# Kernel optimization log

Measured on AMD Instinct MI355X. Metric: run time of the kernel, lower is better.

The kernel has to match this reference:

```python
import jax, jax.numpy as jnp
import numpy as np

MAX_GRAD = 200.0
N_BLOCKS = 8

@jax.custom_jvp
def sqrt_bound(x):
    return jnp.sqrt(x)

@sqrt_bound.defjvp
def _sqrt_bound_jvp(primals, tangents):
    (x,), (xd,) = primals, tangents
    clipped = jnp.maximum(x, 1.0 / (4.0 * MAX_GRAD * MAX_GRAD))
    return jnp.sqrt(x), xd / (2.0 * jnp.sqrt(clipped))

def block_diag_linear(x, W, b):
    # x: [B,S,Din], W: [n_blocks, Din/n, Dout/n], b: [Dout]
    B, S, Din = x.shape
    n, blk_in, blk_out = W.shape
    xb = x.reshape(B, S, n, blk_in)
    y = jnp.einsum('bsnh,nhd->bsnd', xb, W).reshape(B, S, n * blk_out)
    return y + b

def _scan_combine(c1, c2):
    a1r, a1i, x1r, x1i = c1
    a2r, a2i, x2r, x2i = c2
    ar = a2r * a1r - a2i * a1i
    ai = a2r * a1i + a2i * a1r
    xr = a2r * x1r - a2i * x1i + x2r
    xi = a2r * x1i + a2i * x1r + x2i
    return (ar, ai, xr, xi)

def rglru_forward(x, a_real_param, a_imag_param, W_in, b_in, Wg_x, bg_x, Wg_a, bg_a, W_out, b_out):
    # x: [B, S, d_in]
    x_h = jnp.einsum('bsd,dh->bsh', x, W_in) + b_in          # [B,S,d_hidden]
    gate_x = jax.nn.sigmoid(block_diag_linear(x_h, Wg_x, bg_x))  # [B,S,Dh]
    gate_a = jax.nn.sigmoid(block_diag_linear(x_h, Wg_a, bg_a))  # [B,S,Dh]
    log_a = -8.0 * gate_a * jax.nn.softplus(a_real_param)        # Re(log a)
    log_a_imag = a_imag_param * gate_a                           # Im(log a)
    mag = jnp.exp(log_a)
    a_re = mag * jnp.cos(log_a_imag)
    a_im = mag * jnp.sin(log_a_imag)
    a_sq = jnp.exp(2.0 * log_a)                                  # |a|^2
    Dh = log_a.shape[-1]
    # merged_to_complex: first half -> real part, second half -> imag part
    xr = x_h[..., :Dh]
    xi = x_h[..., Dh:]
    xr = gate_x * xr
    xi = gate_x * xi
    norm = sqrt_bound(1.0 - a_sq)                                # input normalization
    xr = norm * xr
    xi = norm * xi
    # linear recurrence h_t = a_t * h_{t-1} + x_t  (h0 = 0), parallel scan over seq axis
    _, _, hr, hi = jax.lax.associative_scan(_scan_combine, (a_re, a_im, xr, xi), axis=1)
    h = jnp.concatenate([hr, hi], axis=-1)                       # complex_to_merged
    h_last = jnp.concatenate([hr[:, -1], hi[:, -1]], axis=-1)    # [B, d_hidden]
    y = jnp.einsum('bsh,hd->bsd', h, W_out) + b_out              # Dense(d_in)
    return y, h_last

def setup_inputs() -> dict:
    key = jax.random.key(0)
    ks = jax.random.split(key, 10)
    B, S, d_in, d_hidden = 4, 4096, 2048, 2048
    Dh = d_hidden // 2
    blk_in, blk_out = d_hidden // N_BLOCKS, Dh // N_BLOCKS
    r_min, r_max, max_imag, eps = 0.9, 0.999, 0.1, 1e-8
    u1 = jax.random.uniform(ks[0], (Dh,))
    a_real = 0.5 * jnp.log(u1 * (r_max**2 - r_min**2) + r_min**2 + eps)
    a_real_param = jnp.log(jnp.exp(-a_real) - 1.0)
    a_imag_param = jnp.pi * max_imag * jax.random.uniform(ks[1], (Dh,))
    x = jax.random.normal(ks[2], (B, S, d_in), dtype=jnp.float32)
    W_in = jax.random.normal(ks[3], (d_in, d_hidden)) / np.sqrt(d_in)
    Wg_x = jax.random.normal(ks[4], (N_BLOCKS, blk_in, blk_out)) / np.sqrt(blk_in)
    Wg_a = jax.random.normal(ks[5], (N_BLOCKS, blk_in, blk_out)) / np.sqrt(blk_in)
    W_out = jax.random.normal(ks[6], (d_hidden, d_in)) / np.sqrt(d_hidden)
    return {
        'x': x,
        'a_real_param': a_real_param.astype(jnp.float32),
        'a_imag_param': a_imag_param.astype(jnp.float32),
        'W_in': W_in.astype(jnp.float32), 'b_in': jnp.zeros((d_hidden,), jnp.float32),
        'Wg_x': Wg_x.astype(jnp.float32), 'bg_x': jnp.zeros((Dh,), jnp.float32),
        'Wg_a': Wg_a.astype(jnp.float32), 'bg_a': jnp.zeros((Dh,), jnp.float32),
        'W_out': W_out.astype(jnp.float32), 'b_out': jnp.zeros((d_in,), jnp.float32),
    }

def reference(x, a_real_param, a_imag_param, W_in, b_in, Wg_x, bg_x, Wg_a, bg_a, W_out, b_out):
    return rglru_forward(x, a_real_param, a_imag_param, W_in, b_in, Wg_x, bg_x, Wg_a, bg_a, W_out, b_out)
```

## Files before the change

kernel.cpp:

```cpp
#include <hip/hip_runtime.h>
#include <hip/hip_bf16.h>


typedef unsigned short u16;
typedef unsigned int u32;
typedef __attribute__((ext_vector_type(8))) short short8;
typedef __attribute__((ext_vector_type(4))) float floatx4;

#define DEV __device__ __forceinline__

DEV float bf2f(u16 u) { union { u32 i; float f; } v; v.i = ((u32)u) << 16; return v.f; }
DEV u16 f2bf(float f) {
  union { float f; u32 i; } v; v.f = f;
  u32 r = v.i + 0x7fffu + ((v.i >> 16) & 1u);
  return (u16)(r >> 16);
}
DEV float sigmoidf_(float x) { return 1.f / (1.f + __expf(-x)); }

template <typename T> DEV T toOut(float v);
template <> DEV u16 toOut<u16>(float v) { return f2bf(v); }
template <> DEV float toOut<float>(float v) { return v; }

#if __has_builtin(__builtin_amdgcn_global_load_lds)
#define USE_ASYNC_LDS 1
#endif

DEV void cp16(const void* g, void* l) {
#if defined(USE_ASYNC_LDS) && defined(__HIP_DEVICE_COMPILE__)
  __builtin_amdgcn_global_load_lds((const __attribute__((address_space(1))) u32*)g,
                                   (__attribute__((address_space(3))) u32*)l, 16, 0, 0);
#else
  *(short8*)l = *(const short8*)g;
#endif
}
#define WAIT_VM() asm volatile("s_waitcnt vmcnt(0)" ::: "memory")

__global__ __launch_bounds__(256) void convert_f32_bf16(
    const float* __restrict__ src, u16* __restrict__ dst, long n) {
  long i = ((long)blockIdx.x * 256 + threadIdx.x) * 8;
  if (i >= n) return;
  float4 a = *(const float4*)(src + i);
  float4 b = *(const float4*)(src + i + 4);
  union { u16 u[8]; short8 v; } o;
  o.u[0] = f2bf(a.x); o.u[1] = f2bf(a.y); o.u[2] = f2bf(a.z); o.u[3] = f2bf(a.w);
  o.u[4] = f2bf(b.x); o.u[5] = f2bf(b.y); o.u[6] = f2bf(b.z); o.u[7] = f2bf(b.w);
  *(short8*)(dst + i) = o.v;
}

__global__ __launch_bounds__(256) void transpose_f32_bf16(
    const float* __restrict__ src, u16* __restrict__ dst, int R, int C,
    long sBatch, long dBatch) {
  __shared__ u16 tile[32][33];
  const int n = blockIdx.z;
  src += (long)n * sBatch;
  dst += (long)n * dBatch;
  const int c0 = blockIdx.x * 32, r0 = blockIdx.y * 32;
  const int tx = threadIdx.x, ty = threadIdx.y;
#pragma unroll
  for (int i = 0; i < 32; i += 8)
    tile[ty + i][tx] = f2bf(src[(long)(r0 + ty + i) * C + c0 + tx]);
  __syncthreads();
#pragma unroll
  for (int i = 0; i < 32; i += 8) dst[(long)(c0 + ty + i) * R + r0 + tx] = tile[tx][ty + i];
}

template <typename OutT>
__global__ __launch_bounds__(256) void gemm_bt_bias(
    const u16* __restrict__ A, const u16* __restrict__ BT,
    const float* __restrict__ bias, OutT* __restrict__ C, int M, int N, int K) {
  __shared__ __align__(16) u16 As[128 * 64];
  __shared__ __align__(16) u16 Bs[128 * 64];
  const int mt = M >> 7;
  const int bm = blockIdx.x % mt, bn = blockIdx.x / mt;
  const int m0 = bm << 7, n0 = bn << 7;
  const int tid = threadIdx.x;
  const int lane = tid & 63, wid = tid >> 6;
  const int wm = (wid & 1) << 6, wn = (wid >> 1) << 6;
  const int lq = lane >> 4, lm = lane & 15;

  floatx4 acc[4][4];
#pragma unroll
  for (int i = 0; i < 4; ++i)
#pragma unroll
    for (int j = 0; j < 4; ++j) { acc[i][j].x = 0.f; acc[i][j].y = 0.f; acc[i][j].z = 0.f; acc[i][j].w = 0.f; }

  for (int kt = 0; kt < K; kt += 64) {
#pragma unroll
    for (int j = 0; j < 4; ++j) {
      int slot = (j << 8) + tid;
      int row = slot >> 3, ch = slot & 7;
      int gch = ch ^ (row & 7);
      cp16(A + (size_t)(m0 + row) * K + kt + (gch << 3), (char*)As + slot * 16);
    }
#pragma unroll
    for (int j = 0; j < 4; ++j) {
      int slot = (j << 8) + tid;
      int row = slot >> 3, ch = slot & 7;
      int gch = ch ^ (row & 7);
      cp16(BT + (size_t)(n0 + row) * K + kt + (gch << 3), (char*)Bs + slot * 16);
    }
    WAIT_VM();
    __syncthreads();
#pragma unroll
    for (int kk = 0; kk < 64; kk += 32) {
      const int lc = (kk >> 3) + lq;
      short8 af[4], bfr[4];
#pragma unroll
      for (int mi = 0; mi < 4; ++mi) {
        int r = wm + mi * 16 + lm;
        af[mi] = *(const short8*)&As[r * 64 + ((lc ^ (r & 7)) << 3)];
      }
#pragma unroll
      for (int ni = 0; ni < 4; ++ni) {
        int r = wn + ni * 16 + lm;
        bfr[ni] = *(const short8*)&Bs[r * 64 + ((lc ^ (r & 7)) << 3)];
      }
#pragma unroll
      for (int mi = 0; mi < 4; ++mi)
#pragma unroll
        for (int ni = 0; ni < 4; ++ni)
          acc[mi][ni] = __builtin_amdgcn_mfma_f32_16x16x32_bf16(af[mi], bfr[ni], acc[mi][ni], 0, 0, 0);
    }
    __syncthreads();
  }
#pragma unroll
  for (int ni = 0; ni < 4; ++ni) {
    int col = n0 + wn + ni * 16 + lm;
    float bv = bias[col];
#pragma unroll
    for (int mi = 0; mi < 4; ++mi) {
      int rbase = m0 + wm + mi * 16 + lq * 4;
#pragma unroll
      for (int r = 0; r < 4; ++r)
        C[(size_t)(rbase + r) * N + col] = toOut<OutT>(acc[mi][ni][r] + bv);
    }
  }
}

__global__ __launch_bounds__(256, 2) void gate_elem_kernel(
    const u16* __restrict__ xh, const u16* __restrict__ wgt,
    const float* __restrict__ bgx, const float* __restrict__ bga,
    const float* __restrict__ arp,
    float* __restrict__ ga_out, u16* __restrict__ xr_out, u16* __restrict__ xi_out) {
  __shared__ __align__(16) u16 As[128 * 64];
  __shared__ __align__(16) u16 Bs[256 * 64];

  const int m0 = blockIdx.x << 7;
  const int blk = blockIdx.y;
  const int tid = threadIdx.x;
  const int lane = tid & 63, wid = tid >> 6;
  const int wm = (wid & 1) << 6, wn = (wid >> 1) << 6;
  const int lq = lane >> 4, lm = lane & 15;

  floatx4 acc[4][8];
#pragma unroll
  for (int i = 0; i < 4; ++i)
#pragma unroll
    for (int j = 0; j < 8; ++j) { acc[i][j].x = 0.f; acc[i][j].y = 0.f; acc[i][j].z = 0.f; acc[i][j].w = 0.f; }

  const u16* Ag = xh + (size_t)m0 * 2048 + blk * 256;
  const u16* Bg = wgt + (size_t)blk * 65536;

  for (int kt = 0; kt < 256; kt += 64) {
#pragma unroll
    for (int j = 0; j < 4; ++j) {
      int slot = (j << 8) + tid;
      int row = slot >> 3, ch = slot & 7;
      int gch = ch ^ (row & 7);
      cp16(Ag + (size_t)row * 2048 + kt + (gch << 3), (char*)As + slot * 16);
    }
#pragma unroll
    for (int j = 0; j < 8; ++j) {
      int slot = (j << 8) + tid;
      int row = slot >> 3, ch = slot & 7;
      int gch = ch ^ (row & 7);
      cp16(Bg + (size_t)row * 256 + kt + (gch << 3), (char*)Bs + slot * 16);
    }
    WAIT_VM();
    __syncthreads();
#pragma unroll
    for (int kk = 0; kk < 64; kk += 32) {
      const int lc = (kk >> 3) + lq;
      short8 af[4], bfr[8];
#pragma unroll
      for (int mi = 0; mi < 4; ++mi) {
        int r = wm + mi * 16 + lm;
        af[mi] = *(const short8*)&As[r * 64 + ((lc ^ (r & 7)) << 3)];
      }
#pragma unroll
      for (int ni = 0; ni < 8; ++ni) {
        int r = (ni < 4) ? (wn + ni * 16 + lm) : (128 + wn + (ni - 4) * 16 + lm);
        bfr[ni] = *(const short8*)&Bs[r * 64 + ((lc ^ (r & 7)) << 3)];
      }
#pragma unroll
      for (int mi = 0; mi < 4; ++mi)
#pragma unroll
        for (int ni = 0; ni < 8; ++ni)
          acc[mi][ni] = __builtin_amdgcn_mfma_f32_16x16x32_bf16(af[mi], bfr[ni], acc[mi][ni], 0, 0, 0);
    }
    __syncthreads();
  }

#pragma unroll
  for (int ni = 0; ni < 4; ++ni) {
    const int c = (blk << 7) + wn + ni * 16 + lm;
    const float bxv = bgx[c], bav = bga[c];
    const float sp = log1pf(__expf(arp[c]));
#pragma unroll
    for (int mi = 0; mi < 4; ++mi) {
      const size_t rowg0 = (size_t)m0 + wm + mi * 16 + lq * 4;
#pragma unroll
      for (int r = 0; r < 4; ++r) {
        const size_t rowg = rowg0 + r;
        float gxv = sigmoidf_(acc[mi][ni][r] + bxv);
        float gav = sigmoidf_(acc[mi][ni + 4][r] + bav);
        float mag = __expf(-8.f * gav * sp);
        float norm = sqrtf(fmaxf(1.f - mag * mag, 0.f));
        float f = norm * gxv;
        ga_out[rowg * 1024 + c] = gav;
        xr_out[rowg * 1024 + c] = f2bf(f * bf2f(xh[rowg * 2048 + c]));
        xi_out[rowg * 1024 + c] = f2bf(f * bf2f(xh[rowg * 2048 + 1024 + c]));
      }
    }
  }
}

__global__ __launch_bounds__(256) void scan_pass1(
    const float* __restrict__ ga, const u16* __restrict__ xr, const u16* __restrict__ xi,
    const float* __restrict__ arp, const float* __restrict__ aip,
    float* __restrict__ Ar, float* __restrict__ Ai,
    float* __restrict__ Xr, float* __restrict__ Xi) {
  int tid = blockIdx.x * 256 + threadIdx.x;
  int c = tid & 1023;
  int chunk = (tid >> 10) & 63;
  int b = tid >> 16;
  float sp = log1pf(__expf(arp[c]));
  float aim = aip[c];
  size_t base = ((size_t)b * 4096 + chunk * 64) * 1024 + c;
  float Arr = 1.f, Aii = 0.f, Xrr = 0.f, Xii = 0.f;
#pragma unroll 4
  for (int i = 0; i < 64; ++i) {
    size_t idx = base + (size_t)i * 1024;
    float g = ga[idx];
    float mag = __expf(-8.f * g * sp);
    float s, co;
    __sincosf(aim * g, &s, &co);
    float ar = mag * co, ai = mag * s;
    float nxr = ar * Xrr - ai * Xii + bf2f(xr[idx]);
    float nxi = ar * Xii + ai * Xrr + bf2f(xi[idx]);
    Xrr = nxr; Xii = nxi;
    float nar = ar * Arr - ai * Aii;
    float nai = ar * Aii + ai * Arr;
    Arr = nar; Aii = nai;
  }
  Ar[tid] = Arr; Ai[tid] = Aii; Xr[tid] = Xrr; Xi[tid] = Xii;
}

__global__ __launch_bounds__(256) void scan_pass2(
    const float* __restrict__ Ar, const float* __restrict__ Ai,
    const float* __restrict__ Xr, const float* __restrict__ Xi,
    float* __restrict__ Hr, float* __restrict__ Hi) {
  int tid = blockIdx.x * 256 + threadIdx.x;
  int c = tid & 1023, b = tid >> 10;
  float hr = 0.f, hi = 0.f;
  for (int j = 0; j < 64; ++j) {
    int idx = (b << 16) + (j << 10) + c;
    Hr[idx] = hr; Hi[idx] = hi;
    float ar = Ar[idx], ai = Ai[idx];
    float nhr = ar * hr - ai * hi + Xr[idx];
    float nhi = ar * hi + ai * hr + Xi[idx];
    hr = nhr; hi = nhi;
  }
}

__global__ __launch_bounds__(256) void scan_pass3(
    const float* __restrict__ ga, const u16* __restrict__ xr, const u16* __restrict__ xi,
    const float* __restrict__ arp, const float* __restrict__ aip,
    const float* __restrict__ Hr, const float* __restrict__ Hi,
    u16* __restrict__ h_out, float* __restrict__ tail) {
  int tid = blockIdx.x * 256 + threadIdx.x;
  int c = tid & 1023;
  int chunk = (tid >> 10) & 63;
  int b = tid >> 16;
  float sp = log1pf(__expf(arp[c]));
  float aim = aip[c];
  size_t row0 = (size_t)b * 4096 + chunk * 64;
  size_t base = row0 * 1024 + c;
  float hr = Hr[tid], hi = Hi[tid];
#pragma unroll 4
  for (int i = 0; i < 64; ++i) {
    size_t idx = base + (size_t)i * 1024;
    float g = ga[idx];
    float mag = __expf(-8.f * g * sp);
    float s, co;
    __sincosf(aim * g, &s, &co);
    float ar = mag * co, ai = mag * s;
    float nhr = ar * hr - ai * hi + bf2f(xr[idx]);
    float nhi = ar * hi + ai * hr + bf2f(xi[idx]);
    hr = nhr; hi = nhi;
    size_t r = row0 + i;
    h_out[r * 2048 + c] = f2bf(hr);
    h_out[r * 2048 + 1024 + c] = f2bf(hi);
  }
  if (chunk == 63) {
    tail[(size_t)b * 2048 + c] = hr;
    tail[(size_t)b * 2048 + 1024 + c] = hi;
  }
}

static const size_t OFF_XH = 0;
static const size_t OFF_GA = 67108864;
static const size_t OFF_XR = 134217728;
static const size_t OFF_XI = 167772160;
static const size_t OFF_WIT = 201326592;
static const size_t OFF_WOT = 209715200;
static const size_t OFF_WGT = 218103808;
static const size_t OFF_AGR = 219152384;
static const size_t OFF_AGI = 220200960;
static const size_t OFF_AXR = 221249536;
static const size_t OFF_AXI = 222298112;
static const size_t OFF_HPR = 223346688;
static const size_t OFF_HPI = 224395264;

extern "C" void kernel_launch(void* const* d_in, const int* in_sizes, int n_in,
                              void* d_out, int out_size, void* d_ws, size_t ws_size,
                              hipStream_t stream) {
  const float* x    = (const float*)d_in[0];
  const float* arp  = (const float*)d_in[1];
  const float* aip  = (const float*)d_in[2];
  const float* W_in = (const float*)d_in[3];
  const float* b_in = (const float*)d_in[4];
  const float* Wg_x = (const float*)d_in[5];
  const float* bg_x = (const float*)d_in[6];
  const float* Wg_a = (const float*)d_in[7];
  const float* bg_a = (const float*)d_in[8];
  const float* W_out = (const float*)d_in[9];
  const float* b_out = (const float*)d_in[10];

  char* ws = (char*)d_ws;
  u16* XH = (u16*)(ws + OFF_XH);
  u16* XB = (u16*)(ws + OFF_GA);
  float* GA = (float*)(ws + OFF_GA);
  u16* XR = (u16*)(ws + OFF_XR);
  u16* XI = (u16*)(ws + OFF_XI);
  u16* WIT = (u16*)(ws + OFF_WIT);
  u16* WOT = (u16*)(ws + OFF_WOT);
  u16* WGT = (u16*)(ws + OFF_WGT);
  float* AGR = (float*)(ws + OFF_AGR);
  float* AGI = (float*)(ws + OFF_AGI);
  float* AXR = (float*)(ws + OFF_AXR);
  float* AXI = (float*)(ws + OFF_AXI);
  float* HPR = (float*)(ws + OFF_HPR);
  float* HPI = (float*)(ws + OFF_HPI);

  float* y_out = (float*)d_out;
  float* h_last = (float*)d_out + (size_t)16384 * 2048;

  convert_f32_bf16<<<16384, 256, 0, stream>>>(x, XB, (long)16384 * 2048);

  dim3 tb(32, 8);
  transpose_f32_bf16<<<dim3(64, 64, 1), tb, 0, stream>>>(W_in, WIT, 2048, 2048, 0, 0);
  transpose_f32_bf16<<<dim3(64, 64, 1), tb, 0, stream>>>(W_out, WOT, 2048, 2048, 0, 0);
  transpose_f32_bf16<<<dim3(4, 8, 8), tb, 0, stream>>>(Wg_x, WGT, 256, 128, 32768, 65536);
  transpose_f32_bf16<<<dim3(4, 8, 8), tb, 0, stream>>>(Wg_a, WGT + 32768, 256, 128, 32768, 65536);

  gemm_bt_bias<u16><<<2048, 256, 0, stream>>>(XB, WIT, b_in, XH, 16384, 2048, 2048);
  gate_elem_kernel<<<dim3(128, 8), 256, 0, stream>>>(XH, WGT, bg_x, bg_a, arp, GA, XR, XI);
  scan_pass1<<<1024, 256, 0, stream>>>(GA, XR, XI, arp, aip, AGR, AGI, AXR, AXI);
  scan_pass2<<<16, 256, 0, stream>>>(AGR, AGI, AXR, AXI, HPR, HPI);
  scan_pass3<<<1024, 256, 0, stream>>>(GA, XR, XI, arp, aip, HPR, HPI, XH , h_last);
  gemm_bt_bias<float><<<2048, 256, 0, stream>>>(XH, WOT, b_out, y_out, 16384, 2048, 2048);
}
```

Before: 832.2 us.

## Replace 128x128 GEMM with double-buffered 256x256 tile pipelined kernel

Replaces the two large dense GEMMs with a 512-thread kernel that computes 256x256 output tiles. It double-buffers LDS, stages async loads a quarter-tile ahead interleaved with MFMA quadrants, and raises MFMA priority with s_setprio. It also swizzles block-to-tile mapping across XCDs and writes the epilogue through LDS for vectorized coalesced stores. This targets load latency stalls and low operand reuse in the old single-buffered kernel, at the cost of 128KB LDS per block, higher register pressure, and fragile hand-tuned waitcnt/barrier ordering.

```diff
diff --git a/kernel.cpp b/kernel.cpp
--- a/kernel.cpp
+++ b/kernel.cpp
@@ -4,6 +4,7 @@
 
 typedef unsigned short u16;
 typedef unsigned int u32;
+typedef unsigned long long u64;
 typedef __attribute__((ext_vector_type(8))) short short8;
 typedef __attribute__((ext_vector_type(4))) float floatx4;
 
@@ -16,10 +17,6 @@
   return (u16)(r >> 16);
 }
 DEV float sigmoidf_(float x) { return 1.f / (1.f + __expf(-x)); }
-
-template <typename T> DEV T toOut(float v);
-template <> DEV u16 toOut<u16>(float v) { return f2bf(v); }
-template <> DEV float toOut<float>(float v) { return v; }
 
 #if __has_builtin(__builtin_amdgcn_global_load_lds)
 #define USE_ASYNC_LDS 1
@@ -64,75 +61,155 @@
   for (int i = 0; i < 32; i += 8) dst[(long)(c0 + ty + i) * R + r0 + tx] = tile[tx][ty + i];
 }
 
+#define MQ(MH, NH)                                                                   \
+  {                                                                                  \
+    _Pragma("unroll") for (int mi = 0; mi < 4; ++mi)                                 \
+        _Pragma("unroll") for (int nj = 0; nj < 2; ++nj) {                           \
+      acc[(MH)*4 + mi][(NH)*2 + nj] = __builtin_amdgcn_mfma_f32_16x16x32_bf16(       \
+          af[(MH)*4 + mi][0], bf[(NH)*2 + nj][0], acc[(MH)*4 + mi][(NH)*2 + nj],     \
+          0, 0, 0);                                                                  \
+      acc[(MH)*4 + mi][(NH)*2 + nj] = __builtin_amdgcn_mfma_f32_16x16x32_bf16(       \
+          af[(MH)*4 + mi][1], bf[(NH)*2 + nj][1], acc[(MH)*4 + mi][(NH)*2 + nj],     \
+          0, 0, 0);                                                                  \
+    }                                                                                \
+  }
+
+#define AOFF(mi, k2) ((((wr << 7) + ((mi) << 4) + lm) << 6) + (((((k2) << 2) + lq) ^ sz) << 3))
+#define BOFF(nj, k2) ((((wc << 6) + ((nj) << 4) + lm) << 6) + (((((k2) << 2) + lq) ^ sz) << 3))
+
 template <typename OutT>
-__global__ __launch_bounds__(256) void gemm_bt_bias(
+__global__ __launch_bounds__(512, 2) void gemm256_bt_bias(
     const u16* __restrict__ A, const u16* __restrict__ BT,
     const float* __restrict__ bias, OutT* __restrict__ C, int M, int N, int K) {
-  __shared__ __align__(16) u16 As[128 * 64];
-  __shared__ __align__(16) u16 Bs[128 * 64];
-  const int mt = M >> 7;
-  const int bm = blockIdx.x % mt, bn = blockIdx.x / mt;
-  const int m0 = bm << 7, n0 = bn << 7;
+  __shared__ __align__(16) u16 As[2 * 16384];
+  __shared__ __align__(16) u16 Bs[2 * 16384];
+  const int mt = M >> 8;
+  const int cpx = gridDim.x >> 3;
+  const int bid = blockIdx.x;
+  const int wg = (bid & 7) * cpx + (bid >> 3);
+  const int bm = wg % mt, bn = wg / mt;
+  const int m0 = bm << 8, n0 = bn << 8;
   const int tid = threadIdx.x;
   const int lane = tid & 63, wid = tid >> 6;
-  const int wm = (wid & 1) << 6, wn = (wid >> 1) << 6;
+  const int wr = wid >> 2, wc = wid & 3;
   const int lq = lane >> 4, lm = lane & 15;
-
-  floatx4 acc[4][4];
-#pragma unroll
-  for (int i = 0; i < 4; ++i)
+  const int sz = lm & 7;
+  const int NT = K >> 6;
+
+  auto stage = [&](int h) {
+    int t = h >> 2, j = h & 3;
+    const u16* src;
+    u16* dst;
+    if (j < 2) { src = A + (size_t)(m0 + (j << 7)) * K; dst = As; }
+    else       { src = BT + (size_t)(n0 + ((j & 1) << 7)) * K; dst = Bs; }
+    dst += ((t & 1) << 14) + ((j & 1) << 13);
+    const size_t kb = (size_t)(t << 6);
+#pragma unroll
+    for (int l = 0; l < 2; ++l) {
+      int slot = (l << 9) + tid;
+      int row = slot >> 3;
+      int gch = (slot & 7) ^ (row & 7);
+      cp16(src + (size_t)row * K + kb + (gch << 3), (char*)dst + slot * 16);
+    }
+  };
+
+  floatx4 acc[8][4];
+#pragma unroll
+  for (int i = 0; i < 8; ++i)
 #pragma unroll
     for (int j = 0; j < 4; ++j) { acc[i][j].x = 0.f; acc[i][j].y = 0.f; acc[i][j].z = 0.f; acc[i][j].w = 0.f; }
-
-  for (int kt = 0; kt < K; kt += 64) {
-#pragma unroll
-    for (int j = 0; j < 4; ++j) {
-      int slot = (j << 8) + tid;
-      int row = slot >> 3, ch = slot & 7;
-      int gch = ch ^ (row & 7);
-      cp16(A + (size_t)(m0 + row) * K + kt + (gch << 3), (char*)As + slot * 16);
-    }
-#pragma unroll
-    for (int j = 0; j < 4; ++j) {
-      int slot = (j << 8) + tid;
-      int row = slot >> 3, ch = slot & 7;
-      int gch = ch ^ (row & 7);
-      cp16(BT + (size_t)(n0 + row) * K + kt + (gch << 3), (char*)Bs + slot * 16);
-    }
-    WAIT_VM();
+  short8 af[8][2], bf[4][2];
+
+#pragma unroll
+  for (int h = 0; h < 7; ++h)
+    if (h < 4 * NT) stage(h);
+  asm volatile("s_waitcnt vmcnt(6)" ::: "memory");
+  __builtin_amdgcn_s_barrier();
+
+  for (int T = 0; T < NT; ++T) {
+    const u16* Asb = As + ((T & 1) << 14);
+    const u16* Bsb = Bs + ((T & 1) << 14);
+    const int hb = (T << 2) + 7;
+#pragma unroll
+    for (int mi = 0; mi < 8; ++mi) {
+      af[mi][0] = *(const short8*)(Asb + AOFF(mi, 0));
+      af[mi][1] = *(const short8*)(Asb + AOFF(mi, 1));
+    }
+#pragma unroll
+    for (int nj = 0; nj < 2; ++nj) {
+      bf[nj][0] = *(const short8*)(Bsb + BOFF(nj, 0));
+      bf[nj][1] = *(const short8*)(Bsb + BOFF(nj, 1));
+    }
+    if (hb < 4 * NT) stage(hb);
+    __builtin_amdgcn_s_barrier();
+    asm volatile("s_waitcnt lgkmcnt(0)" ::: "memory");
+    __builtin_amdgcn_sched_barrier(0);
+    __builtin_amdgcn_s_setprio(1);
+    MQ(0, 0);
+    __builtin_amdgcn_s_setprio(0);
+    __builtin_amdgcn_s_barrier();
+#pragma unroll
+    for (int nj = 2; nj < 4; ++nj) {
+      bf[nj][0] = *(const short8*)(Bsb + BOFF(nj, 0));
+      bf[nj][1] = *(const short8*)(Bsb + BOFF(nj, 1));
+    }
+    if (hb + 1 < 4 * NT) stage(hb + 1);
+    __builtin_amdgcn_s_barrier();
+    asm volatile("s_waitcnt lgkmcnt(0)" ::: "memory");
+    __builtin_amdgcn_sched_barrier(0);
+    __builtin_amdgcn_s_setprio(1);
+    MQ(0, 1);
+    __builtin_amdgcn_s_setprio(0);
+    __builtin_amdgcn_s_barrier();
+    if (hb + 2 < 4 * NT) stage(hb + 2);
+    __builtin_amdgcn_s_barrier();
+    __builtin_amdgcn_s_setprio(1);
+    MQ(1, 0);
+    __builtin_amdgcn_s_setprio(0);
+    __builtin_amdgcn_s_barrier();
+    if (hb + 3 < 4 * NT) stage(hb + 3);
+    __builtin_amdgcn_s_barrier();
+    __builtin_amdgcn_s_setprio(1);
+    MQ(1, 1);
+    __builtin_amdgcn_s_setprio(0);
+    if (T == NT - 2) { asm volatile("s_waitcnt vmcnt(0)" ::: "memory"); }
+    else if (T < NT - 2) { asm volatile("s_waitcnt vmcnt(6)" ::: "memory"); }
+    __builtin_amdgcn_s_barrier();
+  }
+
+  float bv[4];
+#pragma unroll
+  for (int nj = 0; nj < 4; ++nj) bv[nj] = bias[n0 + (wc << 6) + nj * 16 + lm];
+  float* Cs = (float*)As;
+#pragma unroll
+  for (int s = 0; s < 4; ++s) {
     __syncthreads();
-#pragma unroll
-    for (int kk = 0; kk < 64; kk += 32) {
-      const int lc = (kk >> 3) + lq;
-      short8 af[4], bfr[4];
-#pragma unroll
-      for (int mi = 0; mi < 4; ++mi) {
-        int r = wm + mi * 16 + lm;
-        af[mi] = *(const short8*)&As[r * 64 + ((lc ^ (r & 7)) << 3)];
+    if (wr == (s >> 1)) {
+#pragma unroll
+      for (int mi2 = 0; mi2 < 4; ++mi2) {
+        const int mi = ((s & 1) << 2) + mi2;
+#pragma unroll
+        for (int nj = 0; nj < 4; ++nj)
+#pragma unroll
+          for (int rr = 0; rr < 4; ++rr)
+            Cs[(mi2 * 16 + lq * 4 + rr) * 256 + (wc << 6) + nj * 16 + lm] =
+                acc[mi][nj][rr] + bv[nj];
       }
-#pragma unroll
-      for (int ni = 0; ni < 4; ++ni) {
-        int r = wn + ni * 16 + lm;
-        bfr[ni] = *(const short8*)&Bs[r * 64 + ((lc ^ (r & 7)) << 3)];
+    }
+    __syncthreads();
+#pragma unroll
+    for (int w = 0; w < 8; ++w) {
+      int fi = (w << 9) + tid;
+      int rl = fi >> 6, cc = fi & 63;
+      float4 v = *(const float4*)&Cs[rl * 256 + (cc << 2)];
+      size_t grow = (size_t)(m0 + (s << 6) + rl) * N + n0 + (cc << 2);
+      if constexpr (sizeof(OutT) == 2) {
+        union { u16 u[4]; u64 q; } o;
+        o.u[0] = f2bf(v.x); o.u[1] = f2bf(v.y); o.u[2] = f2bf(v.z); o.u[3] = f2bf(v.w);
+        *(u64*)((u16*)C + grow) = o.q;
+      } else {
+        *(float4*)((float*)C + grow) = v;
       }
-#pragma unroll
-      for (int mi = 0; mi < 4; ++mi)
-#pragma unroll
-        for (int ni = 0; ni < 4; ++ni)
-          acc[mi][ni] = __builtin_amdgcn_mfma_f32_16x16x32_bf16(af[mi], bfr[ni], acc[mi][ni], 0, 0, 0);
-    }
-    __syncthreads();
-  }
-#pragma unroll
-  for (int ni = 0; ni < 4; ++ni) {
-    int col = n0 + wn + ni * 16 + lm;
-    float bv = bias[col];
-#pragma unroll
-    for (int mi = 0; mi < 4; ++mi) {
-      int rbase = m0 + wm + mi * 16 + lq * 4;
-#pragma unroll
-      for (int r = 0; r < 4; ++r)
-        C[(size_t)(rbase + r) * N + col] = toOut<OutT>(acc[mi][ni][r] + bv);
     }
   }
 }
@@ -364,10 +441,10 @@
   transpose_f32_bf16<<<dim3(4, 8, 8), tb, 0, stream>>>(Wg_x, WGT, 256, 128, 32768, 65536);
   transpose_f32_bf16<<<dim3(4, 8, 8), tb, 0, stream>>>(Wg_a, WGT + 32768, 256, 128, 32768, 65536);
 
-  gemm_bt_bias<u16><<<2048, 256, 0, stream>>>(XB, WIT, b_in, XH, 16384, 2048, 2048);
+  gemm256_bt_bias<u16><<<512, 512, 0, stream>>>(XB, WIT, b_in, XH, 16384, 2048, 2048);
   gate_elem_kernel<<<dim3(128, 8), 256, 0, stream>>>(XH, WGT, bg_x, bg_a, arp, GA, XR, XI);
   scan_pass1<<<1024, 256, 0, stream>>>(GA, XR, XI, arp, aip, AGR, AGI, AXR, AXI);
   scan_pass2<<<16, 256, 0, stream>>>(AGR, AGI, AXR, AXI, HPR, HPI);
   scan_pass3<<<1024, 256, 0, stream>>>(GA, XR, XI, arp, aip, HPR, HPI, XH , h_last);
-  gemm_bt_bias<float><<<2048, 256, 0, stream>>>(XH, WOT, b_out, y_out, 16384, 2048, 2048);
-}
+  gemm256_bt_bias<float><<<512, 512, 0, stream>>>(XH, WOT, b_out, y_out, 16384, 2048, 2048);
+}
```

New measurement: 731.1 us. -12.1%, faster.
